# Kernel tuning notes

Hardware: AMD Instinct MI355X
Metric: run time of the kernel (lower is better)

## Reference

```python
import jax, jax.numpy as jnp
import numpy as np

N = 100000
E = 1_600_000
D_IN, D_HID, D_OUT = 100, 512, 200
NUM_PATH_AGG = 5   # walks per node in sample_neighbors_and_aggregate
MAX_LEN = 4        # max walk length (incl. start node)
NUM_PATH_FINAL = 10  # global paths in sample_path


def _build_nbr(src, dst, n):
    """Padded neighbor table [n, max_deg] (int32) + degree vector [n]."""
    deg = np.zeros(n, np.int64)
    np.add.at(deg, src, 1)
    maxd = max(int(deg.max()), 1)
    nbr = np.zeros((n, maxd), np.int32)
    order = np.argsort(src, kind='stable')
    ssrc, sdst = src[order], dst[order]
    offs = np.zeros(n + 1, np.int64)
    offs[1:] = np.cumsum(deg)
    rank = np.arange(len(ssrc)) - offs[ssrc]
    nbr[ssrc, rank] = sdst
    return jnp.asarray(nbr), jnp.asarray(deg.astype(np.int32))


def setup_inputs() -> dict:
    key = jax.random.key(0)
    ks = jax.random.split(key, 4)
    x = jax.random.normal(ks[0], (N, D_IN), jnp.float32)
    edge_index = jax.random.randint(ks[1], (2, E), 0, N, jnp.int64)
    ei = np.asarray(edge_index)
    src, dst = ei[0], ei[1]
    # directed neighbor list (get_neighbor_list)
    nbr_dir, deg_dir = _build_nbr(src, dst, N)
    # bi-directional neighbor list (reverse edge added unless self-loop)
    m = src != dst
    nbr_bi, deg_bi = _build_nbr(np.concatenate([src, dst[m]]),
                                np.concatenate([dst, src[m]]), N)
    W1 = jax.random.normal(ks[2], (D_HID, D_IN), jnp.float32) * 0.05
    b1 = jnp.zeros((D_HID,), jnp.float32)
    W3 = jax.random.normal(ks[3], (D_OUT, D_HID), jnp.float32) * 0.05
    b3 = jnp.zeros((D_OUT,), jnp.float32)
    return dict(x=x, edge_index=edge_index, nbr_bi=nbr_bi, deg_bi=deg_bi,
                nbr_dir=nbr_dir, deg_dir=deg_dir, W1=W1, b1=b1, W3=W3, b3=b3)


def _random_walk(key, starts, nbr, deg, extra_steps):
    """Vectorized random walks. Returns nodes [L, M], masks [L, M] (bool).
    A step is invalid (walk stopped) once the current node has no neighbors."""
    cur = starts
    valid = jnp.ones(starts.shape, bool)
    nodes, masks = [cur], [valid]
    for j in range(extra_steps):
        u = jax.random.uniform(jax.random.fold_in(key, j), starts.shape)
        d = deg[cur]
        choice = jnp.minimum((u * d.astype(u.dtype)).astype(jnp.int32),
                             jnp.maximum(d - 1, 0))
        valid = valid & (d > 0)
        cur = jnp.where(valid, nbr[cur, choice], cur)
        nodes.append(cur)
        masks.append(valid)
    return jnp.stack(nodes), jnp.stack(masks)


def reference(x, edge_index, nbr_bi, deg_bi, nbr_dir, deg_dir, W1, b1, W3, b3):
    n = x.shape[0]
    kw = jax.random.key(42)
    # out = relu(fc1(x))
    h = jax.nn.relu(x @ W1.T + b1)  # [N, D_HID]

    # sample_neighbors_and_aggregate: 5 walks of length<=4 starting at every node
    starts1 = jnp.tile(jnp.arange(n, dtype=jnp.int32), NUM_PATH_AGG)  # [5N]
    nodes1, masks1 = _random_walk(jax.random.fold_in(kw, 0), starts1,
                                  nbr_bi, deg_bi, MAX_LEN - 1)
    # [L, 5N] -> [L*5, N]; tile concatenates copies so axis split is (L, 5, N)
    entries = nodes1.reshape(MAX_LEN, NUM_PATH_AGG, n).reshape(-1, n)
    mentries = masks1.reshape(MAX_LEN, NUM_PATH_AGG, n).reshape(-1, n)

    def body(carry, sm):
        acc, cnt = carry
        s, m = sm
        acc = acc + jnp.where(m[:, None], h[s], 0.0)  # masked gather [N, D_HID]
        cnt = cnt + m.astype(h.dtype)
        return (acc, cnt), None

    (acc, cnt), _ = jax.lax.scan(
        body, (jnp.zeros_like(h), jnp.zeros((n,), h.dtype)), (entries, mentries))
    agg = acc / cnt[:, None]  # per-node mean over visited nodes (cnt >= 5)

    # out = relu(fc3(agg))
    out2 = jax.nn.relu(agg @ W3.T + b3)  # [N, D_OUT]

    # sample_path: 10 walks from random start nodes on the DIRECTED graph
    starts2 = jax.random.randint(jax.random.fold_in(kw, 1),
                                 (NUM_PATH_FINAL,), 0, n, jnp.int32)
    nodes2, masks2 = _random_walk(jax.random.fold_in(kw, 2), starts2,
                                  nbr_dir, deg_dir, MAX_LEN - 1)
    g = out2[nodes2]                         # [L, 10, D_OUT]
    w = masks2.astype(out2.dtype)            # [L, 10]
    mean = (g * w[..., None]).sum((0, 1)) / w.sum()
    return mean[None, None, :]               # [1, 1, D_OUT] (matches torch keepdims)
```

## Files before the change

### kernel.cpp

```cpp
#include <hip/hip_runtime.h>
#include <stdint.h>
#include <string.h>

#define JAX_THREEFRY_PARTITIONABLE 1

#define DIN 100
#define DHID 512
#define DOUT 200
#define NPATH_AGG 5
#define NFINAL 10
#define MAXLEN 4
#define NSLOT (MAXLEN * NFINAL)
#define NE 16
#define QSPLIT 4
#define NBLK_P1 (NSLOT * QSPLIT)

struct RngConsts {
  uint32_t kA[3][2];
  int      starts2[NFINAL];
  float    u2[3][NFINAL];
  int      N, maxd_bi, maxd_dir;
};

__host__ __device__ inline void tf2x32(uint32_t k0, uint32_t k1,
                                       uint32_t& x0, uint32_t& x1) {
  const uint32_t k2 = k0 ^ k1 ^ 0x1BD11BDAu;
  x0 += k0; x1 += k1;
#define TFR(r) { x0 += x1; x1 = (x1 << (r)) | (x1 >> (32 - (r))); x1 ^= x0; }
  TFR(13) TFR(15) TFR(26) TFR(6)
  x0 += k1; x1 += k2 + 1u;
  TFR(17) TFR(29) TFR(16) TFR(24)
  x0 += k2; x1 += k0 + 2u;
  TFR(13) TFR(15) TFR(26) TFR(6)
  x0 += k0; x1 += k1 + 3u;
  TFR(17) TFR(29) TFR(16) TFR(24)
  x0 += k1; x1 += k2 + 4u;
  TFR(13) TFR(15) TFR(26) TFR(6)
  x0 += k2; x1 += k0 + 5u;
#undef TFR
}

__host__ __device__ inline uint32_t jax_bits32(uint32_t k0, uint32_t k1,
                                               uint32_t idx, uint32_t half) {
#if JAX_THREEFRY_PARTITIONABLE
  (void)half;
  uint32_t x0 = 0u, x1 = idx;
  tf2x32(k0, k1, x0, x1);
  return x0 ^ x1;
#else
  uint32_t x0, x1;
  const bool lo = idx < half;
  if (lo) { x0 = idx;        x1 = idx + half; }
  else    { x0 = idx - half; x1 = idx;        }
  tf2x32(k0, k1, x0, x1);
  return lo ? x0 : x1;
#endif
}

__host__ __device__ inline float bits_to_unif(uint32_t bits) {
  uint32_t f = (bits >> 9) | 0x3F800000u;
  float r;
  memcpy(&r, &f, 4);
  return r - 1.0f;
}

__device__ __forceinline__ void walk_step(const int* __restrict__ nbr,
                                          const int* __restrict__ deg,
                                          int maxd, int lane, float u,
                                          int& cur, int& valid) {
  const int d = deg[cur];
  const long long base = (long long)cur * maxd;
  int r0 = 0, r1 = 0, r2 = 0, r3 = 0;
  if (lane < maxd)       r0 = nbr[base + lane];
  if (lane + 64 < maxd)  r1 = nbr[base + lane + 64];
  if (lane + 128 < maxd) r2 = nbr[base + lane + 128];
  if (lane + 192 < maxd) r3 = nbr[base + lane + 192];
  int c = (int)(u * (float)d);
  const int cm = (d - 1 > 0) ? (d - 1) : 0;
  if (c > cm) c = cm;
  const int cl = c & 63;
  const int v0 = __shfl(r0, cl);
  const int v1 = __shfl(r1, cl);
  const int v2 = __shfl(r2, cl);
  const int v3 = __shfl(r3, cl);
  int v = (c < 64) ? v0 : (c < 128) ? v1 : (c < 192) ? v2 : v3;
  if (c >= 256) v = nbr[base + c];
  valid = valid && (d > 0);
  if (valid) cur = v;
}

__global__ __launch_bounds__(512) void k_slot(
    const float* __restrict__ x,
    const int* __restrict__ nbr_bi, const int* __restrict__ deg_bi,
    const int* __restrict__ nbr_dir, const int* __restrict__ deg_dir,
    const float* __restrict__ W1, const float* __restrict__ b1,
    RngConsts rc, int* __restrict__ maskArr, float* __restrict__ aggAll) {
  __shared__ int   vnode[NE];
  __shared__ int   vmask[NE];
  __shared__ float xs[NE][DIN];

  const int bid = blockIdx.x;
  const int tid = threadIdx.x;
  const int wv = tid >> 6, lane = tid & 63;
  const int slot = bid >> 2, q = bid & (QSPLIT - 1);
  const int w = slot % NFINAL, j = slot / NFINAL;

  int cur = rc.starts2[w];
  int valid = 1;
  for (int t = 0; t < j; ++t)
    walk_step(nbr_dir, deg_dir, rc.maxd_dir, lane, rc.u2[t][w], cur, valid);

  if (q == 0 && tid == 0) maskArr[slot] = valid;
  if (!valid) return;

  const int n = cur;
  if (tid == 0) { vnode[0] = n; vmask[0] = 1; }
  if (wv < NPATH_AGG) {
    const uint32_t wkr = (uint32_t)(wv * rc.N + n);
    int c2 = n, v2 = 1;
#pragma unroll
    for (int jj = 0; jj < MAXLEN - 1; ++jj) {
      const float u = bits_to_unif(
          jax_bits32(rc.kA[jj][0], rc.kA[jj][1], wkr, 250000u));
      walk_step(nbr_bi, deg_bi, rc.maxd_bi, lane, u, c2, v2);
      if (lane == 0) {
        vnode[1 + jj * NPATH_AGG + wv] = c2;
        vmask[1 + jj * NPATH_AGG + wv] = v2;
      }
    }
  }
  __syncthreads();

  for (int idx = tid; idx < NE * DIN; idx += 512) {
    const int e = idx / DIN, k = idx % DIN;
    xs[e][k] = x[(long long)vnode[e] * DIN + k];
  }
  __syncthreads();

  const int usub = tid >> 2, ks = tid & 3;
  const int unit = q * 128 + usub;
  const float4* __restrict__ w1r = (const float4*)(W1 + (long long)unit * DIN);
  float acc[NE];
#pragma unroll
  for (int e = 0; e < NE; ++e) acc[e] = 0.0f;
  for (int k4 = ks; k4 < DIN / 4; k4 += 4) {
    const float4 wv4 = w1r[k4];
#pragma unroll
    for (int e = 0; e < NE; ++e) {
      const float4 xv = *(const float4*)(&xs[e][k4 * 4]);
      acc[e] += wv4.x * xv.x + wv4.y * xv.y + wv4.z * xv.z + wv4.w * xv.w;
    }
  }
#pragma unroll
  for (int e = 0; e < NE; ++e) {
    float p = acc[e];
    p += __shfl_xor(p, 1);
    p += __shfl_xor(p, 2);
    acc[e] = p;
  }
  if (ks == 0) {
    float cntf = 5.0f;
#pragma unroll
    for (int e = 1; e < NE; ++e) cntf += (float)vmask[e];
    const float bb = b1[unit];
    float h0 = acc[0] + bb;
    h0 = (h0 > 0.0f) ? h0 : 0.0f;
    float hs = 5.0f * h0;
#pragma unroll
    for (int e = 1; e < NE; ++e) {
      if (vmask[e]) {
        const float hv = acc[e] + bb;
        hs += (hv > 0.0f) ? hv : 0.0f;
      }
    }
    aggAll[(long long)slot * DHID + unit] = hs / cntf;
  }
}

__global__ __launch_bounds__(256) void k_fc3(
    const float* __restrict__ W3, const float* __restrict__ b3,
    const int* __restrict__ maskArr, const float* __restrict__ aggAll,
    float* __restrict__ out) {
  __shared__ int   maskS[NSLOT];
  __shared__ float partial[4];

  const int o = blockIdx.x;
  const int tid = threadIdx.x;
  const int wv = tid >> 6, lane = tid & 63;

  if (tid < NSLOT) maskS[tid] = maskArr[tid];
  __syncthreads();

  const float4* __restrict__ w4 = (const float4*)(W3 + (long long)o * DHID);
  const float4 g0 = w4[lane];
  const float4 g1 = w4[64 + lane];
  const float b3o = b3[o];

  float acc = 0.0f;
  for (int s = wv; s < NSLOT; s += 4) {
    if (maskS[s]) {
      const float4* a4 = (const float4*)(aggAll + (long long)s * DHID);
      const float4 a0 = a4[lane];
      const float4 a1 = a4[64 + lane];
      float p = a0.x * g0.x + a0.y * g0.y + a0.z * g0.z + a0.w * g0.w
              + a1.x * g1.x + a1.y * g1.y + a1.z * g1.z + a1.w * g1.w;
#pragma unroll
      for (int off = 32; off; off >>= 1) p += __shfl_xor(p, off);
      const float r = p + b3o;
      acc += (r > 0.0f) ? r : 0.0f;
    }
  }
  if (lane == 0) partial[wv] = acc;
  __syncthreads();
  if (tid == 0) {
    float wsum = 0.0f;
    for (int s = 0; s < NSLOT; ++s) wsum += (float)maskS[s];
    out[o] = (partial[0] + partial[1] + partial[2] + partial[3]) / wsum;
  }
}

static void h_enc(const uint32_t k[2], uint32_t x0, uint32_t x1, uint32_t out[2]) {
  tf2x32(k[0], k[1], x0, x1);
  out[0] = x0; out[1] = x1;
}
static void h_foldin(const uint32_t k[2], uint32_t data, uint32_t out[2]) {
  h_enc(k, 0u, data, out);
}

extern "C" void kernel_launch(void* const* d_in, const int* in_sizes, int n_in,
                              void* d_out, int out_size, void* d_ws, size_t ws_size,
                              hipStream_t stream) {
  const float* x       = (const float*)d_in[0];
  const int*   nbr_bi  = (const int*)d_in[2];
  const int*   deg_bi  = (const int*)d_in[3];
  const int*   nbr_dir = (const int*)d_in[4];
  const int*   deg_dir = (const int*)d_in[5];
  const float* W1      = (const float*)d_in[6];
  const float* b1      = (const float*)d_in[7];
  const float* W3      = (const float*)d_in[8];
  const float* b3      = (const float*)d_in[9];

  const int N = in_sizes[0] / DIN;
  RngConsts rc;
  rc.N = N;
  rc.maxd_bi  = in_sizes[2] / N;
  rc.maxd_dir = in_sizes[4] / N;

  const uint32_t kw[2] = {0u, 42u};
  uint32_t kA[2];
  h_foldin(kw, 0u, kA);
  for (uint32_t j = 0; j < 3; ++j) h_foldin(kA, j, rc.kA[j]);

  uint32_t kS[2];
  h_foldin(kw, 1u, kS);
  uint32_t k1_[2], k2_[2];
#if JAX_THREEFRY_PARTITIONABLE
  h_enc(kS, 0u, 0u, k1_);
  h_enc(kS, 0u, 1u, k2_);
#else
  {
    uint32_t a[2], b[2];
    h_enc(kS, 0u, 2u, a);
    h_enc(kS, 1u, 3u, b);
    k1_[0] = a[0]; k1_[1] = b[0];
    k2_[0] = a[1]; k2_[1] = b[1];
  }
#endif
  {
    const uint32_t span = (uint32_t)N;
    uint32_t mult = 65536u % span;
    mult = (uint32_t)(mult * mult) % span;
    for (uint32_t i = 0; i < NFINAL; ++i) {
      const uint32_t hi = jax_bits32(k1_[0], k1_[1], i, NFINAL / 2);
      const uint32_t lo = jax_bits32(k2_[0], k2_[1], i, NFINAL / 2);
      uint32_t off = (hi % span) * mult + (lo % span);
      off %= span;
      rc.starts2[i] = (int)off;
    }
  }

  uint32_t kP[2];
  h_foldin(kw, 2u, kP);
  for (uint32_t j = 0; j < 3; ++j) {
    uint32_t kPj[2];
    h_foldin(kP, j, kPj);
    for (uint32_t i = 0; i < NFINAL; ++i)
      rc.u2[j][i] = bits_to_unif(jax_bits32(kPj[0], kPj[1], i, NFINAL / 2));
  }

  int*   maskArr = (int*)d_ws;
  float* aggAll  = (float*)(maskArr + NSLOT);

  k_slot<<<NBLK_P1, 512, 0, stream>>>(x, nbr_bi, deg_bi, nbr_dir, deg_dir,
                                      W1, b1, rc, maskArr, aggAll);
  k_fc3<<<DOUT, 256, 0, stream>>>(W3, b3, maskArr, aggAll, (float*)d_out);
}
```

Before: 21.50 us.

## Stage walk rows during walks, split hidden units over more blocks, widen fc3

Each walking wavefront now copies its visited node's x row into shared memory right after every step, and a spare wave loads the start node's row. This removes the separate gather loop and one barrier. Hidden units are split across 8 blocks per slot instead of 4, with 8 threads per unit doing the K reduction, which doubles block count and cuts per-thread FMA work. The fc3 kernel uses 512 threads with 8 waves and an unrolled slot loop. In exchange, each slot's random walks are recomputed redundantly in twice as many blocks.

After: 19.80 us, median of 2. -7.9%, faster.

```diff
diff --git a/kernel.cpp b/kernel.cpp
--- a/kernel.cpp
+++ b/kernel.cpp
@@ -12,7 +12,7 @@
 #define MAXLEN 4
 #define NSLOT (MAXLEN * NFINAL)
 #define NE 16
-#define QSPLIT 4
+#define QSPLIT 8
 #define NBLK_P1 (NSLOT * QSPLIT)
 
 struct RngConsts {
@@ -89,20 +89,28 @@
   if (valid) cur = v;
 }
 
+__device__ __forceinline__ void stage_row(const float* __restrict__ x,
+                                          float* __restrict__ dst,
+                                          int node, int lane) {
+  if (lane < DIN / 2) {
+    *(float2*)(dst + lane * 2) =
+        *(const float2*)(x + (long long)node * DIN + lane * 2);
+  }
+}
+
 __global__ __launch_bounds__(512) void k_slot(
     const float* __restrict__ x,
     const int* __restrict__ nbr_bi, const int* __restrict__ deg_bi,
     const int* __restrict__ nbr_dir, const int* __restrict__ deg_dir,
     const float* __restrict__ W1, const float* __restrict__ b1,
     RngConsts rc, int* __restrict__ maskArr, float* __restrict__ aggAll) {
-  __shared__ int   vnode[NE];
   __shared__ int   vmask[NE];
   __shared__ float xs[NE][DIN];
 
   const int bid = blockIdx.x;
   const int tid = threadIdx.x;
   const int wv = tid >> 6, lane = tid & 63;
-  const int slot = bid >> 2, q = bid & (QSPLIT - 1);
+  const int slot = bid >> 3, q = bid & (QSPLIT - 1);
   const int w = slot % NFINAL, j = slot / NFINAL;
 
   int cur = rc.starts2[w];
@@ -114,7 +122,8 @@
   if (!valid) return;
 
   const int n = cur;
-  if (tid == 0) { vnode[0] = n; vmask[0] = 1; }
+  if (tid == 0) vmask[0] = 1;
+
   if (wv < NPATH_AGG) {
     const uint32_t wkr = (uint32_t)(wv * rc.N + n);
     int c2 = n, v2 = 1;
@@ -123,27 +132,22 @@
       const float u = bits_to_unif(
           jax_bits32(rc.kA[jj][0], rc.kA[jj][1], wkr, 250000u));
       walk_step(nbr_bi, deg_bi, rc.maxd_bi, lane, u, c2, v2);
-      if (lane == 0) {
-        vnode[1 + jj * NPATH_AGG + wv] = c2;
-        vmask[1 + jj * NPATH_AGG + wv] = v2;
-      }
-    }
+      const int ent = 1 + jj * NPATH_AGG + wv;
+      if (lane == 0) vmask[ent] = v2;
+      stage_row(x, &xs[ent][0], c2, lane);
+    }
+  } else if (wv == 5) {
+    stage_row(x, &xs[0][0], n, lane);
   }
   __syncthreads();
 
-  for (int idx = tid; idx < NE * DIN; idx += 512) {
-    const int e = idx / DIN, k = idx % DIN;
-    xs[e][k] = x[(long long)vnode[e] * DIN + k];
-  }
-  __syncthreads();
-
-  const int usub = tid >> 2, ks = tid & 3;
-  const int unit = q * 128 + usub;
+  const int usub = tid >> 3, ks = tid & 7;
+  const int unit = q * 64 + usub;
   const float4* __restrict__ w1r = (const float4*)(W1 + (long long)unit * DIN);
   float acc[NE];
 #pragma unroll
   for (int e = 0; e < NE; ++e) acc[e] = 0.0f;
-  for (int k4 = ks; k4 < DIN / 4; k4 += 4) {
+  for (int k4 = ks; k4 < DIN / 4; k4 += 8) {
     const float4 wv4 = w1r[k4];
 #pragma unroll
     for (int e = 0; e < NE; ++e) {
@@ -156,6 +160,7 @@
     float p = acc[e];
     p += __shfl_xor(p, 1);
     p += __shfl_xor(p, 2);
+    p += __shfl_xor(p, 4);
     acc[e] = p;
   }
   if (ks == 0) {
@@ -177,12 +182,12 @@
   }
 }
 
-__global__ __launch_bounds__(256) void k_fc3(
+__global__ __launch_bounds__(512) void k_fc3(
     const float* __restrict__ W3, const float* __restrict__ b3,
     const int* __restrict__ maskArr, const float* __restrict__ aggAll,
     float* __restrict__ out) {
   __shared__ int   maskS[NSLOT];
-  __shared__ float partial[4];
+  __shared__ float partial[8];
 
   const int o = blockIdx.x;
   const int tid = threadIdx.x;
@@ -197,7 +202,9 @@
   const float b3o = b3[o];
 
   float acc = 0.0f;
-  for (int s = wv; s < NSLOT; s += 4) {
+#pragma unroll
+  for (int i = 0; i < NSLOT / 8; ++i) {
+    const int s = wv + i * 8;
     if (maskS[s]) {
       const float4* a4 = (const float4*)(aggAll + (long long)s * DHID);
       const float4 a0 = a4[lane];
@@ -215,7 +222,10 @@
   if (tid == 0) {
     float wsum = 0.0f;
     for (int s = 0; s < NSLOT; ++s) wsum += (float)maskS[s];
-    out[o] = (partial[0] + partial[1] + partial[2] + partial[3]) / wsum;
+    float tot = 0.0f;
+#pragma unroll
+    for (int v = 0; v < 8; ++v) tot += partial[v];
+    out[o] = tot / wsum;
   }
 }
 
@@ -293,5 +303,5 @@
 
   k_slot<<<NBLK_P1, 512, 0, stream>>>(x, nbr_bi, deg_bi, nbr_dir, deg_dir,
                                       W1, b1, rc, maskArr, aggAll);
-  k_fc3<<<DOUT, 256, 0, stream>>>(W3, b3, maskArr, aggAll, (float*)d_out);
-}
+  k_fc3<<<DOUT, 512, 0, stream>>>(W3, b3, maskArr, aggAll, (float*)d_out);
+}
```
